# Kernel tuning notes

Measured on AMD Instinct MI355X. Metric: run time of the kernel, lower is better.

## Reference

```python
import jax, jax.numpy as jnp
import numpy as np

D_POINTS, D_MODEL, K, B, N = 64, 128, 16, 2, 16384


def _linear(x, w, b=None):
    y = x @ w.T
    return y if b is None else y + b


def setup_inputs() -> dict:
    key = jax.random.key(0)
    ks = jax.random.split(key, 16)
    s = 0.02
    inp = {
        "new_xyz": jax.random.normal(ks[0], (B, N, 3), jnp.float32),
        "grouped_xyz": jax.random.normal(ks[1], (B, 3, N, K), jnp.float32),
        "grouped_idx": jax.random.randint(ks[2], (B, N, K), 0, N),
        "features": jax.random.normal(ks[3], (B, N, D_POINTS), jnp.float32),
        "fc1_w": jax.random.normal(ks[4], (D_MODEL, D_POINTS), jnp.float32) * s,
        "fc1_b": jnp.zeros((D_MODEL,), jnp.float32),
        "wq": jax.random.normal(ks[5], (D_MODEL, D_MODEL), jnp.float32) * s,
        "wk": jax.random.normal(ks[6], (D_MODEL, D_MODEL), jnp.float32) * s,
        "wv": jax.random.normal(ks[7], (D_MODEL, D_MODEL), jnp.float32) * s,
        "delta_w1": jax.random.normal(ks[8], (D_MODEL, 3), jnp.float32) * s,
        "delta_b1": jnp.zeros((D_MODEL,), jnp.float32),
        "delta_w2": jax.random.normal(ks[9], (D_MODEL, D_MODEL), jnp.float32) * s,
        "delta_b2": jnp.zeros((D_MODEL,), jnp.float32),
        "gamma_w1": jax.random.normal(ks[10], (D_MODEL, D_MODEL), jnp.float32) * s,
        "gamma_b1": jnp.zeros((D_MODEL,), jnp.float32),
        "gamma_w2": jax.random.normal(ks[11], (D_MODEL, D_MODEL), jnp.float32) * s,
        "gamma_b2": jnp.zeros((D_MODEL,), jnp.float32),
    }
    return inp


def reference(new_xyz, grouped_xyz, grouped_idx, features,
              fc1_w, fc1_b, wq, wk, wv,
              delta_w1, delta_b1, delta_w2, delta_b2,
              gamma_w1, gamma_b1, gamma_w2, gamma_b2):
    # x: [B,N,d_model]
    x = _linear(features, fc1_w, fc1_b)
    q = x @ wq.T                               # [B,N,d]
    kx = x @ wk.T                              # [B,N,d]
    vx = x @ wv.T                              # [B,N,d]
    gather = jax.vmap(lambda a, i: a[i])       # per-batch gather -> [B,N,K,d]
    k = gather(kx, grouped_idx)
    v = gather(vx, grouped_idx)
    # pos_enc: fc_delta(new_xyz[:,:,None] - grouped_xyz.permute(0,2,3,1))
    rel = new_xyz[:, :, None, :] - jnp.transpose(grouped_xyz, (0, 2, 3, 1))  # [B,N,K,3]
    pos_enc = _linear(jax.nn.relu(_linear(rel, delta_w1, delta_b1)), delta_w2, delta_b2)
    # attn: fc_gamma(q - k + pos_enc), softmax over neighbor axis
    h = q[:, :, None, :] - k + pos_enc
    attn = _linear(jax.nn.relu(_linear(h, gamma_w1, gamma_b1)), gamma_w2, gamma_b2)
    attn = jax.nn.softmax(attn / np.sqrt(D_MODEL).astype(np.float32), axis=-2)
    out = jnp.einsum('bmnf,bmnf->bmf', attn, v + pos_enc)
    return out
```

## Files before the change

kernel.cpp:

```cpp
#include <hip/hip_runtime.h>
#include <hip/hip_bf16.h>
#include <math.h>

#define BB   2
#define NPTS 16384
#define KNB  16
#define DPTS 64
#define DM   128

typedef float  f32x4  __attribute__((ext_vector_type(4)));
typedef short  bf16x8 __attribute__((ext_vector_type(8)));

__device__ __forceinline__ unsigned short f2bf(float f) {
    union { __hip_bfloat16 h; unsigned short u; } v;
    v.h = __float2bfloat16(f);
    return v.u;
}
__device__ __forceinline__ float bf2f(unsigned short h) {
    union { unsigned u; float f; } v; v.u = ((unsigned)h) << 16;
    return v.f;
}

__device__ __forceinline__ int swz(int row, int col) {
    return row * DM + (col ^ ((row & 7) << 3));
}

#define WOFF_DW2  0
#define WOFF_GW1  16384
#define WOFF_GW2  32768
#define WOFF_WQ   49152
#define WOFF_WK   65536
#define WOFF_WV   81920
#define WOFF_FC1  98304
#define WTOT      106496

__global__ __launch_bounds__(256) void cvtw_kernel(
    const float* __restrict__ dw2, const float* __restrict__ gw1,
    const float* __restrict__ gw2, const float* __restrict__ wq,
    const float* __restrict__ wk, const float* __restrict__ wv,
    const float* __restrict__ fc1_w, unsigned short* __restrict__ wb)
{
    const int i = blockIdx.x * 256 + threadIdx.x;
    if (i >= WTOT) return;
    float v;
    if (i < WOFF_WQ) {
        const int which = i >> 14, off = i & 16383;
        v = (which == 0) ? dw2[off] : (which == 1) ? gw1[off] : gw2[off];
    } else if (i < WOFF_FC1) {
        const int j = i - WOFF_WQ;
        const int which = j >> 14, off = j & 16383;
        v = (which == 0) ? wq[off] : (which == 1) ? wk[off] : wv[off];
    } else {
        v = fc1_w[i - WOFF_FC1];
    }
    wb[i] = f2bf(v);
}

__device__ __forceinline__ void mfma_gemm(const unsigned short* __restrict__ AB,
                                          const unsigned short* __restrict__ Wb,
                                          int lane, int wbase, f32x4 acc[4][2])
{
    const int c = lane & 15, g = lane >> 4;
    bf16x8 Bf[2][4];
#pragma unroll
    for (int ct = 0; ct < 2; ++ct)
#pragma unroll
        for (int ks = 0; ks < 4; ++ks)
            Bf[ct][ks] = *(const bf16x8*)&Wb[(wbase + ct * 16 + c) * DM + ks * 32 + g * 8];
#pragma unroll
    for (int rt = 0; rt < 4; ++rt) {
        bf16x8 Af[4];
#pragma unroll
        for (int ks = 0; ks < 4; ++ks)
            Af[ks] = *(const bf16x8*)&AB[swz(rt * 16 + c, ks * 32 + g * 8)];
#pragma unroll
        for (int ct = 0; ct < 2; ++ct)
#pragma unroll
            for (int ks = 0; ks < 4; ++ks)
                acc[rt][ct] = __builtin_amdgcn_mfma_f32_16x16x32_bf16(
                    Af[ks], Bf[ct][ks], acc[rt][ct], 0, 0, 0);
    }
}

#define P_MT  64
#define FSTR  72

__global__ __launch_bounds__(256, 4) void proj_kernel(
    const float* __restrict__ features, const float* __restrict__ fc1_b,
    const unsigned short* __restrict__ wbf,
    unsigned short* __restrict__ qws, unsigned short* __restrict__ kvws)
{
    __shared__ __align__(16) unsigned short FB[P_MT * FSTR];
    __shared__ __align__(16) unsigned short XB[P_MT * DM];

    const int tid  = threadIdx.x;
    const int lane = tid & 63;
    const int wave = tid >> 6;
    const int wbase = wave * 32;
    const int c  = lane & 15;
    const int g  = lane >> 4;
    const int g4 = g * 4;
    const size_t gp0 = (size_t)blockIdx.x * P_MT;

    for (int i = tid; i < P_MT * 8; i += 256) {
        const int r = i >> 3, o = i & 7;
        const float4 a = *(const float4*)&features[(gp0 + r) * DPTS + o * 8];
        const float4 b = *(const float4*)&features[(gp0 + r) * DPTS + o * 8 + 4];
        bf16x8 t;
        t[0] = (short)f2bf(a.x); t[1] = (short)f2bf(a.y);
        t[2] = (short)f2bf(a.z); t[3] = (short)f2bf(a.w);
        t[4] = (short)f2bf(b.x); t[5] = (short)f2bf(b.y);
        t[6] = (short)f2bf(b.z); t[7] = (short)f2bf(b.w);
        *(bf16x8*)&FB[r * FSTR + o * 8] = t;
    }
    __syncthreads();

    {
        const unsigned short* fw = wbf + WOFF_FC1;
        const float b0 = fc1_b[wbase + c], b1 = fc1_b[wbase + 16 + c];
        f32x4 acc[4][2];
#pragma unroll
        for (int rt = 0; rt < 4; ++rt) {
            acc[rt][0] = (f32x4)b0;
            acc[rt][1] = (f32x4)b1;
        }
        bf16x8 Bf[2][2];
#pragma unroll
        for (int ct = 0; ct < 2; ++ct)
#pragma unroll
            for (int ks = 0; ks < 2; ++ks)
                Bf[ct][ks] = *(const bf16x8*)&fw[(wbase + ct * 16 + c) * DPTS + ks * 32 + g * 8];
#pragma unroll
        for (int rt = 0; rt < 4; ++rt) {
            bf16x8 Af[2];
#pragma unroll
            for (int ks = 0; ks < 2; ++ks)
                Af[ks] = *(const bf16x8*)&FB[(rt * 16 + c) * FSTR + ks * 32 + g * 8];
#pragma unroll
            for (int ct = 0; ct < 2; ++ct)
#pragma unroll
                for (int ks = 0; ks < 2; ++ks)
                    acc[rt][ct] = __builtin_amdgcn_mfma_f32_16x16x32_bf16(
                        Af[ks], Bf[ct][ks], acc[rt][ct], 0, 0, 0);
        }
#pragma unroll
        for (int ct = 0; ct < 2; ++ct) {
            const int col = wbase + ct * 16 + c;
#pragma unroll
            for (int rt = 0; rt < 4; ++rt)
#pragma unroll
                for (int rg = 0; rg < 4; ++rg)
                    XB[swz(rt * 16 + g4 + rg, col)] = f2bf(acc[rt][ct][rg]);
        }
    }
    __syncthreads();

    const unsigned short* wmat[3] = { wbf + WOFF_WQ, wbf + WOFF_WK, wbf + WOFF_WV };
#pragma unroll
    for (int m = 0; m < 3; ++m) {
        f32x4 acc[4][2];
#pragma unroll
        for (int rt = 0; rt < 4; ++rt)
#pragma unroll
            for (int ct = 0; ct < 2; ++ct) acc[rt][ct] = (f32x4)0.f;
        mfma_gemm(XB, wmat[m], lane, wbase, acc);
#pragma unroll
        for (int ct = 0; ct < 2; ++ct) {
            const int col = wbase + ct * 16 + c;
#pragma unroll
            for (int rt = 0; rt < 4; ++rt)
#pragma unroll
                for (int rg = 0; rg < 4; ++rg) {
                    const size_t row = gp0 + rt * 16 + g4 + rg;
                    unsigned short* dst = (m == 0)
                        ? &qws[row * DM + col]
                        : &kvws[row * (2 * DM) + (m == 2 ? DM : 0) + col];
                    *dst = f2bf(acc[rt][ct][rg]);
                }
        }
    }
}

#define K2_PTS 4
#define K2_R   (K2_PTS * KNB)

__global__ __launch_bounds__(256, 4) void attn_kernel(
    const float* __restrict__ new_xyz, const float* __restrict__ grouped_xyz,
    const int* __restrict__ grouped_idx,
    const float* __restrict__ dw1, const float* __restrict__ db1,
    const float* __restrict__ db2,
    const float* __restrict__ gb1, const float* __restrict__ gb2,
    const unsigned short* __restrict__ wbf,
    const unsigned short* __restrict__ qws, const unsigned short* __restrict__ kvws,
    float* __restrict__ out)
{
    __shared__ __align__(16) unsigned short X[K2_R * DM];
    __shared__ float REL[K2_R * 3];
    __shared__ int   IDX[K2_R];

    const int tid  = threadIdx.x;
    const int lane = tid & 63;
    const int wave = tid >> 6;
    const int wbase = wave * 32;
    const int c  = lane & 15;
    const int g  = lane >> 4;
    const int g4 = g * 4;
    const int rr = tid >> 4;
    const int o8 = (tid & 15) * 8;

    const int b   = blockIdx.x / (NPTS / K2_PTS);
    const int m0  = (blockIdx.x % (NPTS / K2_PTS)) * K2_PTS;
    const size_t gp0 = (size_t)b * NPTS + m0;
    const size_t bN  = (size_t)b * NPTS;
    const float SCL = 0.12751743342f;

    const unsigned short* dw2b = wbf + WOFF_DW2;
    const unsigned short* gw1b = wbf + WOFF_GW1;
    const unsigned short* gw2b = wbf + WOFF_GW2;

    float wr[24], bbv[8];
    {
        const float4* wsrc = (const float4*)&dw1[o8 * 3];
#pragma unroll
        for (int t = 0; t < 6; ++t) ((float4*)wr)[t] = wsrc[t];
        const float4* bsrc = (const float4*)&db1[o8];
        ((float4*)bbv)[0] = bsrc[0];
        ((float4*)bbv)[1] = bsrc[1];
    }

    if (tid < K2_R) {
        const int p = tid >> 4, j = tid & 15;
        const size_t m = gp0 + p;
        const int mi = m0 + p;
#pragma unroll
        for (int cc = 0; cc < 3; ++cc)
            REL[tid * 3 + cc] = new_xyz[m * 3 + cc]
                              - grouped_xyz[(((size_t)b * 3 + cc) * NPTS + mi) * KNB + j];
        IDX[tid] = grouped_idx[m * KNB + j];
    }
    __syncthreads();

    bf16x8 q8[4], k8[4];
#pragma unroll
    for (int it = 0; it < 4; ++it) {
        const int r = it * 16 + rr;
        q8[it] = *(const bf16x8*)&qws[(gp0 + it) * DM + o8];
        k8[it] = *(const bf16x8*)&kvws[(bN + IDX[r]) * (2 * DM) + o8];
    }

#pragma unroll
    for (int it = 0; it < 4; ++it) {
        const int r = it * 16 + rr;
        const float rx = REL[r * 3 + 0], ry = REL[r * 3 + 1], rz = REL[r * 3 + 2];
        bf16x8 t;
#pragma unroll
        for (int j = 0; j < 8; ++j) {
            float v = bbv[j];
            v = fmaf(rx, wr[j * 3 + 0], v);
            v = fmaf(ry, wr[j * 3 + 1], v);
            v = fmaf(rz, wr[j * 3 + 2], v);
            t[j] = (short)f2bf(fmaxf(v, 0.f));
        }
        *(bf16x8*)&X[swz(r, o8)] = t;
    }
    __syncthreads();

    f32x4 posr[4][2];
    {
        const float b0 = db2[wbase + c], b1 = db2[wbase + 16 + c];
#pragma unroll
        for (int rt = 0; rt < 4; ++rt) {
            posr[rt][0] = (f32x4)b0;
            posr[rt][1] = (f32x4)b1;
        }
    }
    mfma_gemm(X, dw2b, lane, wbase, posr);
    __syncthreads();
#pragma unroll
    for (int ct = 0; ct < 2; ++ct) {
        const int col = wbase + ct * 16 + c;
#pragma unroll
        for (int rt = 0; rt < 4; ++rt)
#pragma unroll
            for (int rg = 0; rg < 4; ++rg)
                X[swz(rt * 16 + g4 + rg, col)] = f2bf(posr[rt][ct][rg]);
    }
    __syncthreads();

#pragma unroll
    for (int it = 0; it < 4; ++it) {
        const int r = it * 16 + rr;
        const bf16x8 p8 = *(const bf16x8*)&X[swz(r, o8)];
        bf16x8 t;
#pragma unroll
        for (int j = 0; j < 8; ++j) {
            const float hv = bf2f((unsigned short)q8[it][j])
                           - bf2f((unsigned short)k8[it][j])
                           + bf2f((unsigned short)p8[j]);
            t[j] = (short)f2bf(hv);
        }
        *(bf16x8*)&X[swz(r, o8)] = t;
    }
    __syncthreads();

    {
        f32x4 acc[4][2];
        const float b0 = gb1[wbase + c], b1 = gb1[wbase + 16 + c];
#pragma unroll
        for (int rt = 0; rt < 4; ++rt) {
            acc[rt][0] = (f32x4)b0;
            acc[rt][1] = (f32x4)b1;
        }
        mfma_gemm(X, gw1b, lane, wbase, acc);
        __syncthreads();
#pragma unroll
        for (int ct = 0; ct < 2; ++ct) {
            const int col = wbase + ct * 16 + c;
#pragma unroll
            for (int rt = 0; rt < 4; ++rt)
#pragma unroll
                for (int rg = 0; rg < 4; ++rg)
                    X[swz(rt * 16 + g4 + rg, col)] = f2bf(fmaxf(acc[rt][ct][rg], 0.f));
        }
    }
    __syncthreads();

    f32x4 lg[4][2];
#pragma unroll
    for (int rt = 0; rt < 4; ++rt)
#pragma unroll
        for (int ct = 0; ct < 2; ++ct) lg[rt][ct] = (f32x4)0.f;
    mfma_gemm(X, gw2b, lane, wbase, lg);
#pragma unroll
    for (int ct = 0; ct < 2; ++ct) {
        const int col = wbase + ct * 16 + c;
        const float bb = gb2[col];
#pragma unroll
        for (int rt = 0; rt < 4; ++rt)
#pragma unroll
            for (int rg = 0; rg < 4; ++rg)
                lg[rt][ct][rg] = (lg[rt][ct][rg] + bb) * SCL;
    }

#pragma unroll
    for (int rt = 0; rt < 4; ++rt)
#pragma unroll
    for (int ct = 0; ct < 2; ++ct) {
        const int col = wbase + ct * 16 + c;
        f32x4 l = lg[rt][ct];
        float mx = fmaxf(fmaxf(l[0], l[1]), fmaxf(l[2], l[3]));
        mx = fmaxf(mx, __shfl_xor(mx, 16));
        mx = fmaxf(mx, __shfl_xor(mx, 32));
        f32x4 e;
        e[0] = __builtin_amdgcn_exp2f(l[0] - mx);
        e[1] = __builtin_amdgcn_exp2f(l[1] - mx);
        e[2] = __builtin_amdgcn_exp2f(l[2] - mx);
        e[3] = __builtin_amdgcn_exp2f(l[3] - mx);
        float s = e[0] + e[1] + e[2] + e[3];
        s += __shfl_xor(s, 16);
        s += __shfl_xor(s, 32);
        float o = 0.f;
#pragma unroll
        for (int rg = 0; rg < 4; ++rg) {
            const int row = rt * 16 + g4 + rg;
            const float vv = bf2f(kvws[(bN + IDX[row]) * (2 * DM) + DM + col])
                           + posr[rt][ct][rg];
            o = fmaf(e[rg], vv, o);
        }
        o += __shfl_xor(o, 16);
        o += __shfl_xor(o, 32);
        if (g == 0)
            out[(gp0 + rt) * DM + col] = o * __builtin_amdgcn_rcpf(s);
    }
}

extern "C" void kernel_launch(void* const* d_in, const int* in_sizes, int n_in,
                              void* d_out, int out_size, void* d_ws, size_t ws_size,
                              hipStream_t stream)
{
    const float* new_xyz     = (const float*)d_in[0];
    const float* grouped_xyz = (const float*)d_in[1];
    const int*   grouped_idx = (const int*)d_in[2];
    const float* features    = (const float*)d_in[3];
    const float* fc1_w = (const float*)d_in[4];
    const float* fc1_b = (const float*)d_in[5];
    const float* wq    = (const float*)d_in[6];
    const float* wk    = (const float*)d_in[7];
    const float* wv    = (const float*)d_in[8];
    const float* dw1   = (const float*)d_in[9];
    const float* db1   = (const float*)d_in[10];
    const float* dw2   = (const float*)d_in[11];
    const float* db2   = (const float*)d_in[12];
    const float* gw1   = (const float*)d_in[13];
    const float* gb1   = (const float*)d_in[14];
    const float* gw2   = (const float*)d_in[15];
    const float* gb2   = (const float*)d_in[16];
    float* out = (float*)d_out;

    unsigned short* ws = (unsigned short*)d_ws;
    const size_t npt = (size_t)BB * NPTS * DM;
    unsigned short* qws  = ws;
    unsigned short* kvws = ws + npt;
    unsigned short* wbf  = ws + 3 * npt;

    cvtw_kernel<<<(WTOT + 255) / 256, 256, 0, stream>>>(
        dw2, gw1, gw2, wq, wk, wv, fc1_w, wbf);

    proj_kernel<<<(BB * NPTS) / P_MT, 256, 0, stream>>>(
        features, fc1_b, wbf, qws, kvws);

    attn_kernel<<<(BB * NPTS) / K2_PTS, 256, 0, stream>>>(
        new_xyz, grouped_xyz, grouped_idx,
        dw1, db1, db2, gb1, gb2,
        wbf, qws, kvws, out);
}
```

Baseline: 164.6 us.

## Double attention tile to 8 points with 8 waves each owning 16 columns

```diff
diff --git a/kernel.cpp b/kernel.cpp
--- a/kernel.cpp
+++ b/kernel.cpp
@@ -82,6 +82,27 @@
     }
 }
 
+__device__ __forceinline__ void gemm16w(const unsigned short* __restrict__ X,
+                                        const unsigned short* __restrict__ Wb,
+                                        int c, int g, int wb16, f32x4 acc[8])
+{
+    bf16x8 Bf[4];
+#pragma unroll
+    for (int ks = 0; ks < 4; ++ks)
+        Bf[ks] = *(const bf16x8*)&Wb[(wb16 + c) * DM + ks * 32 + g * 8];
+#pragma unroll
+    for (int rt = 0; rt < 8; ++rt) {
+        bf16x8 Af[4];
+#pragma unroll
+        for (int ks = 0; ks < 4; ++ks)
+            Af[ks] = *(const bf16x8*)&X[swz(rt * 16 + c, ks * 32 + g * 8)];
+#pragma unroll
+        for (int ks = 0; ks < 4; ++ks)
+            acc[rt] = __builtin_amdgcn_mfma_f32_16x16x32_bf16(
+                Af[ks], Bf[ks], acc[rt], 0, 0, 0);
+    }
+}
+
 #define P_MT  64
 #define FSTR  72
 
@@ -181,10 +202,10 @@
     }
 }
 
-#define K2_PTS 4
+#define K2_PTS 8
 #define K2_R   (K2_PTS * KNB)
 
-__global__ __launch_bounds__(256, 4) void attn_kernel(
+__global__ __launch_bounds__(512, 4) void attn_kernel(
     const float* __restrict__ new_xyz, const float* __restrict__ grouped_xyz,
     const int* __restrict__ grouped_idx,
     const float* __restrict__ dw1, const float* __restrict__ db1,
@@ -195,18 +216,19 @@
     float* __restrict__ out)
 {
     __shared__ __align__(16) unsigned short X[K2_R * DM];
+    __shared__ __align__(16) unsigned short QB[K2_PTS * DM];
     __shared__ float REL[K2_R * 3];
     __shared__ int   IDX[K2_R];
 
     const int tid  = threadIdx.x;
     const int lane = tid & 63;
     const int wave = tid >> 6;
-    const int wbase = wave * 32;
+    const int wb16 = wave * 16;
     const int c  = lane & 15;
     const int g  = lane >> 4;
     const int g4 = g * 4;
-    const int rr = tid >> 4;
-    const int o8 = (tid & 15) * 8;
+    const int r0e = tid >> 4;
+    const int o8  = (tid & 15) * 8;
 
     const int b   = blockIdx.x / (NPTS / K2_PTS);
     const int m0  = (blockIdx.x % (NPTS / K2_PTS)) * K2_PTS;
@@ -218,83 +240,78 @@
     const unsigned short* gw1b = wbf + WOFF_GW1;
     const unsigned short* gw2b = wbf + WOFF_GW2;
 
-    float wr[24], bbv[8];
+    if (tid < K2_R) {
+        const int p = tid >> 4, j = tid & 15;
+        const size_t m = gp0 + p;
+        const int mi = m0 + p;
+#pragma unroll
+        for (int cc = 0; cc < 3; ++cc)
+            REL[tid * 3 + cc] = new_xyz[m * 3 + cc]
+                              - grouped_xyz[(((size_t)b * 3 + cc) * NPTS + mi) * KNB + j];
+        IDX[tid] = grouped_idx[m * KNB + j];
+    } else if (tid >= 384) {
+        const int i = tid - 384;
+        const int r = i >> 4, o = (i & 15) * 8;
+        *(bf16x8*)&QB[r * DM + o] = *(const bf16x8*)&qws[(gp0 + r) * DM + o];
+    }
+    __syncthreads();
+
+    bf16x8 k8[4];
+#pragma unroll
+    for (int it = 0; it < 4; ++it)
+        k8[it] = *(const bf16x8*)&kvws[(bN + IDX[it * 32 + r0e]) * (2 * DM) + o8];
+
     {
+        float wr[24], bbv[8];
         const float4* wsrc = (const float4*)&dw1[o8 * 3];
 #pragma unroll
         for (int t = 0; t < 6; ++t) ((float4*)wr)[t] = wsrc[t];
         const float4* bsrc = (const float4*)&db1[o8];
         ((float4*)bbv)[0] = bsrc[0];
         ((float4*)bbv)[1] = bsrc[1];
-    }
-
-    if (tid < K2_R) {
-        const int p = tid >> 4, j = tid & 15;
-        const size_t m = gp0 + p;
-        const int mi = m0 + p;
-#pragma unroll
-        for (int cc = 0; cc < 3; ++cc)
-            REL[tid * 3 + cc] = new_xyz[m * 3 + cc]
-                              - grouped_xyz[(((size_t)b * 3 + cc) * NPTS + mi) * KNB + j];
-        IDX[tid] = grouped_idx[m * KNB + j];
-    }
-    __syncthreads();
-
-    bf16x8 q8[4], k8[4];
+#pragma unroll
+        for (int it = 0; it < 4; ++it) {
+            const int r = it * 32 + r0e;
+            const float rx = REL[r * 3 + 0], ry = REL[r * 3 + 1], rz = REL[r * 3 + 2];
+            bf16x8 t;
+#pragma unroll
+            for (int j = 0; j < 8; ++j) {
+                float v = bbv[j];
+                v = fmaf(rx, wr[j * 3 + 0], v);
+                v = fmaf(ry, wr[j * 3 + 1], v);
+                v = fmaf(rz, wr[j * 3 + 2], v);
+                t[j] = (short)f2bf(fmaxf(v, 0.f));
+            }
+            *(bf16x8*)&X[swz(r, o8)] = t;
+        }
+    }
+    __syncthreads();
+
+    f32x4 posr[8];
+    {
+        const float b2v = db2[wb16 + c];
+#pragma unroll
+        for (int rt = 0; rt < 8; ++rt) posr[rt] = (f32x4)b2v;
+    }
+    gemm16w(X, dw2b, c, g, wb16, posr);
+    __syncthreads();
+#pragma unroll
+    for (int rt = 0; rt < 8; ++rt)
+#pragma unroll
+        for (int rg = 0; rg < 4; ++rg)
+            X[swz(rt * 16 + g4 + rg, wb16 + c)] = f2bf(posr[rt][rg]);
+    __syncthreads();
+
 #pragma unroll
     for (int it = 0; it < 4; ++it) {
-        const int r = it * 16 + rr;
-        q8[it] = *(const bf16x8*)&qws[(gp0 + it) * DM + o8];
-        k8[it] = *(const bf16x8*)&kvws[(bN + IDX[r]) * (2 * DM) + o8];
-    }
-
-#pragma unroll
-    for (int it = 0; it < 4; ++it) {
-        const int r = it * 16 + rr;
-        const float rx = REL[r * 3 + 0], ry = REL[r * 3 + 1], rz = REL[r * 3 + 2];
+        const int r = it * 32 + r0e;
+        const int p = r >> 4;
+        const bf16x8 p8 = *(const bf16x8*)&X[swz(r, o8)];
+        const bf16x8 q8 = *(const bf16x8*)&QB[p * DM + o8];
         bf16x8 t;
 #pragma unroll
         for (int j = 0; j < 8; ++j) {
-            float v = bbv[j];
-            v = fmaf(rx, wr[j * 3 + 0], v);
-            v = fmaf(ry, wr[j * 3 + 1], v);
-            v = fmaf(rz, wr[j * 3 + 2], v);
-            t[j] = (short)f2bf(fmaxf(v, 0.f));
-        }
-        *(bf16x8*)&X[swz(r, o8)] = t;
-    }
-    __syncthreads();
-
-    f32x4 posr[4][2];
-    {
-        const float b0 = db2[wbase + c], b1 = db2[wbase + 16 + c];
-#pragma unroll
-        for (int rt = 0; rt < 4; ++rt) {
-            posr[rt][0] = (f32x4)b0;
-            posr[rt][1] = (f32x4)b1;
-        }
-    }
-    mfma_gemm(X, dw2b, lane, wbase, posr);
-    __syncthreads();
-#pragma unroll
-    for (int ct = 0; ct < 2; ++ct) {
-        const int col = wbase + ct * 16 + c;
-#pragma unroll
-        for (int rt = 0; rt < 4; ++rt)
-#pragma unroll
-            for (int rg = 0; rg < 4; ++rg)
-                X[swz(rt * 16 + g4 + rg, col)] = f2bf(posr[rt][ct][rg]);
-    }
-    __syncthreads();
-
-#pragma unroll
-    for (int it = 0; it < 4; ++it) {
-        const int r = it * 16 + rr;
-        const bf16x8 p8 = *(const bf16x8*)&X[swz(r, o8)];
-        bf16x8 t;
-#pragma unroll
-        for (int j = 0; j < 8; ++j) {
-            const float hv = bf2f((unsigned short)q8[it][j])
+            const float hv = bf2f((unsigned short)q8[j])
                            - bf2f((unsigned short)k8[it][j])
                            + bf2f((unsigned short)p8[j]);
             t[j] = (short)f2bf(hv);
@@ -304,50 +321,37 @@
     __syncthreads();
 
     {
-        f32x4 acc[4][2];
-        const float b0 = gb1[wbase + c], b1 = gb1[wbase + 16 + c];
-#pragma unroll
-        for (int rt = 0; rt < 4; ++rt) {
-            acc[rt][0] = (f32x4)b0;
-            acc[rt][1] = (f32x4)b1;
-        }
-        mfma_gemm(X, gw1b, lane, wbase, acc);
+        f32x4 acc[8];
+        const float b1v = gb1[wb16 + c];
+#pragma unroll
+        for (int rt = 0; rt < 8; ++rt) acc[rt] = (f32x4)b1v;
+        gemm16w(X, gw1b, c, g, wb16, acc);
         __syncthreads();
 #pragma unroll
-        for (int ct = 0; ct < 2; ++ct) {
-            const int col = wbase + ct * 16 + c;
-#pragma unroll
-            for (int rt = 0; rt < 4; ++rt)
-#pragma unroll
-                for (int rg = 0; rg < 4; ++rg)
-                    X[swz(rt * 16 + g4 + rg, col)] = f2bf(fmaxf(acc[rt][ct][rg], 0.f));
-        }
-    }
-    __syncthreads();
-
-    f32x4 lg[4][2];
-#pragma unroll
-    for (int rt = 0; rt < 4; ++rt)
-#pragma unroll
-        for (int ct = 0; ct < 2; ++ct) lg[rt][ct] = (f32x4)0.f;
-    mfma_gemm(X, gw2b, lane, wbase, lg);
-#pragma unroll
-    for (int ct = 0; ct < 2; ++ct) {
-        const int col = wbase + ct * 16 + c;
-        const float bb = gb2[col];
-#pragma unroll
-        for (int rt = 0; rt < 4; ++rt)
+        for (int rt = 0; rt < 8; ++rt)
 #pragma unroll
             for (int rg = 0; rg < 4; ++rg)
-                lg[rt][ct][rg] = (lg[rt][ct][rg] + bb) * SCL;
-    }
-
-#pragma unroll
-    for (int rt = 0; rt < 4; ++rt)
-#pragma unroll
-    for (int ct = 0; ct < 2; ++ct) {
-        const int col = wbase + ct * 16 + c;
-        f32x4 l = lg[rt][ct];
+                X[swz(rt * 16 + g4 + rg, wb16 + c)] = f2bf(fmaxf(acc[rt][rg], 0.f));
+    }
+    __syncthreads();
+
+    f32x4 lg[8];
+#pragma unroll
+    for (int rt = 0; rt < 8; ++rt) lg[rt] = (f32x4)0.f;
+    gemm16w(X, gw2b, c, g, wb16, lg);
+    {
+        const float bb = gb2[wb16 + c];
+#pragma unroll
+        for (int rt = 0; rt < 8; ++rt)
+#pragma unroll
+            for (int rg = 0; rg < 4; ++rg)
+                lg[rt][rg] = (lg[rt][rg] + bb) * SCL;
+    }
+
+#pragma unroll
+    for (int rt = 0; rt < 8; ++rt) {
+        const int col = wb16 + c;
+        f32x4 l = lg[rt];
         float mx = fmaxf(fmaxf(l[0], l[1]), fmaxf(l[2], l[3]));
         mx = fmaxf(mx, __shfl_xor(mx, 16));
         mx = fmaxf(mx, __shfl_xor(mx, 32));
@@ -364,7 +368,7 @@
         for (int rg = 0; rg < 4; ++rg) {
             const int row = rt * 16 + g4 + rg;
             const float vv = bf2f(kvws[(bN + IDX[row]) * (2 * DM) + DM + col])
-                           + posr[rt][ct][rg];
+                           + posr[rt][rg];
             o = fmaf(e[rg], vv, o);
         }
         o += __shfl_xor(o, 16);
@@ -409,7 +413,7 @@
     proj_kernel<<<(BB * NPTS) / P_MT, 256, 0, stream>>>(
         features, fc1_b, wbf, qws, kvws);
 
-    attn_kernel<<<(BB * NPTS) / K2_PTS, 256, 0, stream>>>(
+    attn_kernel<<<(BB * NPTS) / K2_PTS, 512, 0, stream>>>(
         new_xyz, grouped_xyz, grouped_idx,
         dw1, db1, db2, gb1, gb2,
         wbf, qws, kvws, out);
```

Result: faster. 155.1 us (-5.8%).
